# Kernel optimization log

Hardware: AMD Instinct MI355X
Metric: run time of the kernel (lower is better)

## Reference

```python
import jax, jax.numpy as jnp
import numpy as np

N_NODES = 50000
N_EDGES = 800000
IN_DIM = 13
HID = 64
LAYER_DIMS = [(IN_DIM, HID), (HID, HID), (HID, HID), (HID, HID), (HID, 1)]


def setup_inputs() -> dict:
    key = jax.random.key(0)
    ks = jax.random.split(key, 20)
    x = jax.random.normal(ks[0], (N_NODES, IN_DIM), dtype=jnp.float32)
    edge_index = jax.random.randint(ks[1], (2, N_EDGES), 0, N_NODES)
    edge_weight = jax.random.uniform(ks[2], (N_EDGES,), dtype=jnp.float32)
    inp = {"x": x, "edge_index": edge_index, "edge_weight": edge_weight}
    for i, (di, do) in enumerate(LAYER_DIMS):
        s = 1.0 / np.sqrt(di)
        inp[f"Wrel{i}"] = (jax.random.normal(ks[3 + 3 * i], (di, do)) * s).astype(jnp.float32)
        inp[f"brel{i}"] = jnp.zeros((do,), dtype=jnp.float32)
        inp[f"Wroot{i}"] = (jax.random.normal(ks[4 + 3 * i], (di, do)) * s).astype(jnp.float32)
    return inp


def _graph_conv(x, src, dst, ew, Wrel, brel, Wroot):
    # PyG GraphConv: out = lin_rel(sum_{j in N(i)} w_e * x_j) + lin_root(x_i)
    msgs = ew[:, None] * x[src]                      # [E, d_in] gather
    aggr = jax.ops.segment_sum(msgs, dst, num_segments=N_NODES)  # [N, d_in]
    return aggr @ Wrel + brel + x @ Wroot


def reference(x, edge_index, edge_weight,
              Wrel0, brel0, Wroot0,
              Wrel1, brel1, Wroot1,
              Wrel2, brel2, Wroot2,
              Wrel3, brel3, Wroot3,
              Wrel4, brel4, Wroot4):
    src, dst = edge_index[0], edge_index[1]  # source_to_target flow
    params = [
        (Wrel0, brel0, Wroot0),
        (Wrel1, brel1, Wroot1),
        (Wrel2, brel2, Wroot2),
        (Wrel3, brel3, Wroot3),
        (Wrel4, brel4, Wroot4),
    ]
    h = x
    for Wr, br, Ws in params[:-1]:
        h = jax.nn.relu(_graph_conv(h, src, dst, edge_weight, Wr, br, Ws))
    Wr, br, Ws = params[-1]
    h = _graph_conv(h, src, dst, edge_weight, Wr, br, Ws)
    return jax.nn.sigmoid(h)  # [N, 1]
```

## Files before the change

### kernel.cpp

```cpp
#include <hip/hip_runtime.h>
#include <math.h>

#define N_NODES 50000
#define N_EDGES 800000
#define NBUCKET 196
#define CHUNK 4096
#define NCHUNK 196
#define SCAN_N (NBUCKET * NCHUNK)
#define SB_A 151
#define SB_B 196
#define EPT 16
#define CAP_FINE 8192
#define MAXEPAD (N_EDGES + N_NODES * 4)

typedef __attribute__((ext_vector_type(8))) _Float16 f16x8;
typedef __attribute__((ext_vector_type(4))) float f32x4;

__device__ __forceinline__ int roundup4(int v) { return (v + 3) & ~3; }


__device__ __forceinline__ int block_excl_scan(int v, int* wsum) {
    int t = threadIdx.x, lane = t & 63, w = t >> 6;
    int sc = v;
    #pragma unroll
    for (int o = 1; o < 64; o <<= 1) {
        int u = __shfl_up(sc, o, 64);
        if (lane >= o) sc += u;
    }
    if (lane == 63) wsum[w] = sc;
    __syncthreads();
    int add = 0;
    #pragma unroll
    for (int j = 0; j < 4; ++j) if (j < w) add += wsum[j];
    return add + sc - v;
}


__global__ void hist_kernel(const int* __restrict__ dst, int* __restrict__ h,
                            int* __restrict__ counts,
                            const float* __restrict__ W1r, const float* __restrict__ W1o,
                            const float* __restrict__ W2r, const float* __restrict__ W2o,
                            const float* __restrict__ W3r, const float* __restrict__ W3o,
                            _Float16* __restrict__ wfrag) {
    if (blockIdx.x >= NCHUNK) {
        int b = blockIdx.x - NCHUNK, t = threadIdx.x;
        const float* Wr = (b == 0) ? W1r : (b == 1) ? W2r : W3r;
        const float* Wo = (b == 0) ? W1o : (b == 1) ? W2o : W3o;
        _Float16* out = wfrag + (size_t)b * 8192;
        for (int i = t; i < 1024; i += 256) {
            int frag = i >> 6, lane = i & 63;
            int m = frag >> 3, ct = (frag >> 1) & 3, ks = frag & 1;
            int col = ct * 16 + (lane & 15);
            int kb = ks * 32 + (lane >> 4) * 8;
            const float* W = m ? Wo : Wr;
            f16x8 v;
            #pragma unroll
            for (int j = 0; j < 8; ++j) v[j] = (_Float16)W[(kb + j) * 64 + col];
            *(f16x8*)&out[(size_t)i * 8] = v;
        }
        return;
    }
    __shared__ int hist[NBUCKET];
    for (int i = threadIdx.x; i < NBUCKET; i += 256) hist[i] = 0;
    __syncthreads();
    int base = blockIdx.x * CHUNK;
    int n = min(CHUNK, N_EDGES - base);
    for (int k = threadIdx.x; k < n; k += 256) {
        int d = dst[base + k];
        atomicAdd(&hist[d >> 8], 1);
        atomicAdd(&counts[d], 1);
    }
    __syncthreads();
    for (int i = threadIdx.x; i < NBUCKET; i += 256)
        h[i * NCHUNK + blockIdx.x] = hist[i];
}


__global__ void scan_blocks_dual(int* __restrict__ h, const int* __restrict__ counts,
                                 int* __restrict__ offs, int* __restrict__ blocksums) {
    __shared__ int wsum[4];
    int bid = blockIdx.x, t = threadIdx.x;
    if (bid < SB_A) {
        int i = bid * 256 + t;
        int v = (i < SCAN_N) ? h[i] : 0;
        int e = block_excl_scan(v, wsum);
        if (i < SCAN_N) h[i] = e;
        if (t == 255) blocksums[bid] = e + v;
    } else {
        int j = (bid - SB_A) * 256 + t;
        int v = (j < N_NODES) ? roundup4(counts[j]) : 0;
        int e = block_excl_scan(v, wsum);
        if (j < N_NODES) offs[j] = e;
        if (t == 255) blocksums[bid] = e + v;
    }
}

__global__ void scan_mid(const int* __restrict__ blocksums, int* __restrict__ blockoffs) {
    __shared__ int wsum[4];
    int base = (blockIdx.x == 0) ? 0 : SB_A;
    int n = (blockIdx.x == 0) ? SB_A : SB_B;
    int t = threadIdx.x;
    int v = (t < n) ? blocksums[base + t] : 0;
    int e = block_excl_scan(v, wsum);
    if (t < n) blockoffs[base + t] = e;
}

__global__ void scan_add_dual(int* __restrict__ h, int* __restrict__ offs,
                              const int* __restrict__ counts,
                              const int* __restrict__ blockoffs) {
    int bid = blockIdx.x, t = threadIdx.x;
    if (bid < SB_A) {
        int i = bid * 256 + t;
        if (i < SCAN_N) h[i] += blockoffs[bid];
    } else {
        int j = (bid - SB_A) * 256 + t;
        if (j < N_NODES) {
            int v = offs[j] + blockoffs[bid];
            offs[j] = v;
            if (j == N_NODES - 1) offs[N_NODES] = v + roundup4(counts[j]);
        }
    }
}


__launch_bounds__(256, 4)
__global__ void scatter_coarse(const int* __restrict__ src, const int* __restrict__ dst,
                               const float* __restrict__ ew, const int* __restrict__ hs,
                               int2* __restrict__ ecoarse) {
    __shared__ int cnt[NBUCKET];
    __shared__ int excl[NBUCKET];
    __shared__ int cur[NBUCKET];
    __shared__ int gbase[NBUCKET];
    __shared__ int wsum[4];
    __shared__ int2 stage[CHUNK];

    int t = threadIdx.x;
    int base = blockIdx.x * CHUNK;
    int n = min(CHUNK, N_EDGES - base);

    for (int i = t; i < NBUCKET; i += 256) {
        cnt[i] = 0;
        gbase[i] = hs[i * NCHUNK + blockIdx.x];
    }
    __syncthreads();

    int rx[EPT];
    float rw[EPT];
    #pragma unroll
    for (int j = 0; j < EPT; ++j) {
        int k = t + j * 256;
        if (k < n) {
            int e = base + k;
            int d = dst[e];
            rx[j] = (d << 16) | src[e];
            rw[j] = ew[e];
            atomicAdd(&cnt[d >> 8], 1);
        }
    }
    __syncthreads();

    {
        int v = (t < NBUCKET) ? cnt[t] : 0;
        int e = block_excl_scan(v, wsum);
        if (t < NBUCKET) { excl[t] = e; cur[t] = e; }
    }
    __syncthreads();

    #pragma unroll
    for (int j = 0; j < EPT; ++j) {
        int k = t + j * 256;
        if (k < n) {
            int b = ((unsigned)rx[j]) >> 24;
            int p = atomicAdd(&cur[b], 1);
            stage[p] = make_int2(rx[j], __float_as_int(rw[j]));
        }
    }
    __syncthreads();

    for (int k = t; k < n; k += 256) {
        int2 r = stage[k];
        int b = ((unsigned)r.x) >> 24;
        ecoarse[gbase[b] + (k - excl[b])] = r;
    }
}


__launch_bounds__(256)
__global__ void fine_sort(const int* __restrict__ h, const int* __restrict__ offs,
                          const int2* __restrict__ ecoarse, int2* __restrict__ esrt) {
    int b = blockIdx.x, t = threadIdx.x;
    __shared__ int cur[256];
    __shared__ int2 stage[CAP_FINE];
    int bstartU = h[b * NCHUNK];
    int bendU = (b == NBUCKET - 1) ? N_EDGES : h[(b + 1) * NCHUNK];
    int nbU = bendU - bstartU;
    int P = offs[b << 8];
    int nodeEnd = min((b + 1) << 8, N_NODES);
    int plen = offs[nodeEnd] - P;
    int dstv = (b << 8) + t;
    cur[t] = (dstv < N_NODES) ? offs[dstv] - P : 0;
    __syncthreads();
    if (plen <= CAP_FINE) {
        for (int k = t; k < plen; k += 256) stage[k] = make_int2(0, 0);
        __syncthreads();
        for (int k = t; k < nbU; k += 256) {
            int2 r = ecoarse[bstartU + k];
            int d = (((unsigned)r.x) >> 16) & 255;
            int p = atomicAdd(&cur[d], 1);
            stage[p] = make_int2(r.x & 0xFFFF, r.y);
        }
        __syncthreads();
        for (int k = t; k < plen; k += 256) esrt[P + k] = stage[k];
    } else {
        for (int k = t; k < plen; k += 256) esrt[P + k] = make_int2(0, 0);
        __syncthreads();
        for (int k = t; k < nbU; k += 256) {
            int2 r = ecoarse[bstartU + k];
            int d = (((unsigned)r.x) >> 16) & 255;
            int p = atomicAdd(&cur[d], 1);
            esrt[P + p] = make_int2(r.x & 0xFFFF, r.y);
        }
    }
}


__device__ __forceinline__ float bcast(float v, int k) {
    return __int_as_float(__builtin_amdgcn_readlane(__float_as_int(v), k));
}


__launch_bounds__(256)
__global__ void layer0_fused(const int* __restrict__ offs, const int2* __restrict__ esrt,
                             const float* __restrict__ x, const float* __restrict__ Wrel,
                             const float* __restrict__ bias, const float* __restrict__ Wroot,
                             _Float16* __restrict__ h0) {
    int wid = (blockIdx.x * blockDim.x + threadIdx.x) >> 6;
    int lane = threadIdx.x & 63;
    float wr[13], wo[13];
    #pragma unroll
    for (int k = 0; k < 13; ++k) {
        wr[k] = Wrel[k * 64 + lane];
        wo[k] = Wroot[k * 64 + lane];
    }
    float bc = bias[lane];
    int q = lane >> 4, f = lane & 15;
    int beg = offs[wid], end = offs[wid + 1];
    float acc = 0.f;
    bool fv = (f < 13);
    int i = beg + q;
    for (; i + 4 < end; i += 8) {
        int2 e0 = esrt[i], e1 = esrt[i + 4];
        float v0 = fv ? x[(size_t)e0.x * 13 + f] : 0.f;
        float v1 = fv ? x[(size_t)e1.x * 13 + f] : 0.f;
        acc = fmaf(__int_as_float(e0.y), v0, acc);
        acc = fmaf(__int_as_float(e1.y), v1, acc);
    }
    if (i < end) {
        int2 e = esrt[i];
        float v = fv ? x[(size_t)e.x * 13 + f] : 0.f;
        acc = fmaf(__int_as_float(e.y), v, acc);
    }
    acc += __shfl_xor(acc, 16, 64);
    acc += __shfl_xor(acc, 32, 64);
    float hv = (lane < 13) ? x[(size_t)wid * 13 + lane] : 0.f;
    float a0 = bc, a1 = 0.f, a2 = 0.f, a3 = 0.f;
    #pragma unroll
    for (int k = 0; k + 2 <= 13; k += 2) {
        a0 = fmaf(bcast(acc, k), wr[k], a0);
        a1 = fmaf(bcast(hv, k), wo[k], a1);
        a2 = fmaf(bcast(acc, k + 1), wr[k + 1], a2);
        a3 = fmaf(bcast(hv, k + 1), wo[k + 1], a3);
    }
    a0 = fmaf(bcast(acc, 12), wr[12], a0);
    a1 = fmaf(bcast(hv, 12), wo[12], a1);
    float o = fmaxf((a0 + a2) + (a1 + a3), 0.f);
    h0[(size_t)wid * 64 + lane] = (_Float16)o;
}


template <bool FINAL>
__launch_bounds__(256)
__global__ void layer_fused(const int* __restrict__ offs, const int2* __restrict__ esrt,
                            const _Float16* __restrict__ hin, const _Float16* __restrict__ wfrag_l,
                            const float* __restrict__ bias, _Float16* __restrict__ hout,
                            const float* __restrict__ Wrel4, const float* __restrict__ Wroot4,
                            float* __restrict__ z, float* __restrict__ root) {
    __shared__ __align__(16) _Float16 aggrHi[32][72];
    __shared__ __align__(16) _Float16 aggrLo[32][72];
    __shared__ float zpart[4][32], rpart[4][32];
    int t = threadIdx.x;
    int rowbase = blockIdx.x * 32;
    int w = t >> 6, lane = t & 63;

    f16x8 br0 = *(const f16x8*)&wfrag_l[(size_t)(((0 * 4 + w) * 2 + 0) * 64 + lane) * 8];
    f16x8 br1 = *(const f16x8*)&wfrag_l[(size_t)(((0 * 4 + w) * 2 + 1) * 64 + lane) * 8];
    f16x8 bo0 = *(const f16x8*)&wfrag_l[(size_t)(((1 * 4 + w) * 2 + 0) * 64 + lane) * 8];
    f16x8 bo1 = *(const f16x8*)&wfrag_l[(size_t)(((1 * 4 + w) * 2 + 1) * 64 + lane) * 8];
    int r = lane & 15, kq = lane >> 4;
    float bc = bias[w * 16 + r];
    float w4rv = 0.f, w4ov = 0.f;
    if (FINAL) { w4rv = Wrel4[w * 16 + r]; w4ov = Wroot4[w * 16 + r]; }

    int qw = t >> 4, l = t & 15;
    int hi8 = l >> 3, f8 = l & 7;
    #pragma unroll
    for (int rr = 0; rr < 2; ++rr) {
        int node = rowbase + qw + rr * 16;
        float a[8] = {0.f, 0.f, 0.f, 0.f, 0.f, 0.f, 0.f, 0.f};
        if (node < N_NODES) {
            int beg = offs[node], end = offs[node + 1];
            int i = beg;
            for (; i + 4 < end; i += 8) {
                int4 p0 = *(const int4*)(esrt + i);
                int4 p1 = *(const int4*)(esrt + i + 2);
                int4 p2 = *(const int4*)(esrt + i + 4);
                int4 p3 = *(const int4*)(esrt + i + 6);
                int s0 = hi8 ? p0.z : p0.x; float w0 = __int_as_float(hi8 ? p0.w : p0.y);
                int s1 = hi8 ? p1.z : p1.x; float w1 = __int_as_float(hi8 ? p1.w : p1.y);
                int s2 = hi8 ? p2.z : p2.x; float w2 = __int_as_float(hi8 ? p2.w : p2.y);
                int s3 = hi8 ? p3.z : p3.x; float w3 = __int_as_float(hi8 ? p3.w : p3.y);
                f16x8 r0 = *(const f16x8*)(hin + (size_t)s0 * 64 + f8 * 8);
                f16x8 r1 = *(const f16x8*)(hin + (size_t)s1 * 64 + f8 * 8);
                f16x8 r2 = *(const f16x8*)(hin + (size_t)s2 * 64 + f8 * 8);
                f16x8 r3 = *(const f16x8*)(hin + (size_t)s3 * 64 + f8 * 8);
                #pragma unroll
                for (int j = 0; j < 8; ++j) {
                    a[j] = fmaf(w0, (float)r0[j], a[j]);
                    a[j] = fmaf(w1, (float)r1[j], a[j]);
                    a[j] = fmaf(w2, (float)r2[j], a[j]);
                    a[j] = fmaf(w3, (float)r3[j], a[j]);
                }
            }
            if (i < end) {
                int4 p0 = *(const int4*)(esrt + i);
                int4 p1 = *(const int4*)(esrt + i + 2);
                int s0 = hi8 ? p0.z : p0.x; float w0 = __int_as_float(hi8 ? p0.w : p0.y);
                int s1 = hi8 ? p1.z : p1.x; float w1 = __int_as_float(hi8 ? p1.w : p1.y);
                f16x8 r0 = *(const f16x8*)(hin + (size_t)s0 * 64 + f8 * 8);
                f16x8 r1 = *(const f16x8*)(hin + (size_t)s1 * 64 + f8 * 8);
                #pragma unroll
                for (int j = 0; j < 8; ++j) {
                    a[j] = fmaf(w0, (float)r0[j], a[j]);
                    a[j] = fmaf(w1, (float)r1[j], a[j]);
                }
            }
        }
        #pragma unroll
        for (int j = 0; j < 8; ++j) a[j] += __shfl_xor(a[j], 8, 64);
        f16x8 wv;
        #pragma unroll
        for (int j = 0; j < 8; ++j) {
            _Float16 hh = (_Float16)a[j];
            wv[j] = hi8 ? (_Float16)(a[j] - (float)hh) : hh;
        }
        int row = qw + rr * 16;
        _Float16* dstp = hi8 ? &aggrLo[row][f8 * 8] : &aggrHi[row][f8 * 8];
        *(f16x8*)dstp = wv;
    }
    __syncthreads();

    #pragma unroll
    for (int g = 0; g < 2; ++g) {
        int lr = g * 16 + r;
        int grow = min(rowbase + lr, N_NODES - 1);
        f32x4 acc = {bc, bc, bc, bc};
        {
            f16x8 Ah = *(const f16x8*)&aggrHi[lr][0 * 32 + kq * 8];
            f16x8 Al = *(const f16x8*)&aggrLo[lr][0 * 32 + kq * 8];
            f16x8 Ar = *(const f16x8*)&hin[(size_t)grow * 64 + 0 * 32 + kq * 8];
            acc = __builtin_amdgcn_mfma_f32_16x16x32_f16(Ah, br0, acc, 0, 0, 0);
            acc = __builtin_amdgcn_mfma_f32_16x16x32_f16(Al, br0, acc, 0, 0, 0);
            acc = __builtin_amdgcn_mfma_f32_16x16x32_f16(Ar, bo0, acc, 0, 0, 0);
        }
        {
            f16x8 Ah = *(const f16x8*)&aggrHi[lr][1 * 32 + kq * 8];
            f16x8 Al = *(const f16x8*)&aggrLo[lr][1 * 32 + kq * 8];
            f16x8 Ar = *(const f16x8*)&hin[(size_t)grow * 64 + 1 * 32 + kq * 8];
            acc = __builtin_amdgcn_mfma_f32_16x16x32_f16(Ah, br1, acc, 0, 0, 0);
            acc = __builtin_amdgcn_mfma_f32_16x16x32_f16(Al, br1, acc, 0, 0, 0);
            acc = __builtin_amdgcn_mfma_f32_16x16x32_f16(Ar, bo1, acc, 0, 0, 0);
        }
        if (FINAL) {
            #pragma unroll
            for (int j = 0; j < 4; ++j) {
                float o = fmaxf(acc[j], 0.f);
                float zz = o * w4rv, rv = o * w4ov;
                #pragma unroll
                for (int m = 1; m < 16; m <<= 1) {
                    zz += __shfl_xor(zz, m, 64);
                    rv += __shfl_xor(rv, m, 64);
                }
                if (r == 0) {
                    int lrow = g * 16 + (lane >> 4) * 4 + j;
                    zpart[w][lrow] = zz;
                    rpart[w][lrow] = rv;
                }
            }
        } else {
            #pragma unroll
            for (int j = 0; j < 4; ++j) {
                int row = rowbase + g * 16 + (lane >> 4) * 4 + j;
                if (row < N_NODES)
                    hout[(size_t)row * 64 + w * 16 + r] = (_Float16)fmaxf(acc[j], 0.f);
            }
        }
    }
    if (FINAL) {
        __syncthreads();
        if (t < 32) {
            int row = rowbase + t;
            if (row < N_NODES) {
                z[row] = zpart[0][t] + zpart[1][t] + zpart[2][t] + zpart[3][t];
                root[row] = rpart[0][t] + rpart[1][t] + rpart[2][t] + rpart[3][t];
            }
        }
    }
}


__launch_bounds__(256)
__global__ void final_aggr(const int* __restrict__ offs, const int2* __restrict__ esrt,
                           const float* __restrict__ z, const float* __restrict__ root,
                           const float* __restrict__ b4, float* __restrict__ out) {
    int tid = blockIdx.x * blockDim.x + threadIdx.x;
    int node = tid >> 2, g = tid & 3;
    if (node >= N_NODES) return;
    int beg = offs[node], end = offs[node + 1];
    float a = 0.f;
    int i = beg + g;
    for (; i + 4 < end; i += 8) {
        int2 e0 = esrt[i], e1 = esrt[i + 4];
        a = fmaf(__int_as_float(e0.y), z[e0.x], a);
        a = fmaf(__int_as_float(e1.y), z[e1.x], a);
    }
    if (i < end) {
        int2 e = esrt[i];
        a = fmaf(__int_as_float(e.y), z[e.x], a);
    }
    a += __shfl_xor(a, 1, 64);
    a += __shfl_xor(a, 2, 64);
    if (g == 0) {
        float v = a + b4[0] + root[node];
        out[node] = 1.f / (1.f + expf(-v));
    }
}


extern "C" void kernel_launch(void* const* d_in, const int* in_sizes, int n_in,
                              void* d_out, int out_size, void* d_ws, size_t ws_size,
                              hipStream_t stream) {
    const float* x = (const float*)d_in[0];
    const int* eidx = (const int*)d_in[1];
    const float* ew = (const float*)d_in[2];
    const float* Wrel[5];
    const float* brel[5];
    const float* Wroot[5];
    for (int i = 0; i < 5; ++i) {
        Wrel[i] = (const float*)d_in[3 + 3 * i];
        brel[i] = (const float*)d_in[4 + 3 * i];
        Wroot[i] = (const float*)d_in[5 + 3 * i];
    }
    const int* src = eidx;
    const int* dst = eidx + N_EDGES;
    float* out = (float*)d_out;

    char* ws = (char*)d_ws;
    size_t off = 0;
    auto alloc = [&](size_t bytes) -> void* {
        void* p = ws + off;
        off = (off + bytes + 255) & ~(size_t)255;
        return p;
    };
    int* h = (int*)alloc((size_t)(SCAN_N + 256) * 4);
    int* blocksums = (int*)alloc(512 * 4);
    int* blockoffs = (int*)alloc(512 * 4);
    int* counts = (int*)alloc((size_t)N_NODES * 4);
    int* offs = (int*)alloc((size_t)(N_NODES + 1) * 4);
    int2* esrt = (int2*)alloc((size_t)MAXEPAD * 8);
    _Float16* h0 = (_Float16*)alloc((size_t)N_NODES * 64 * 2);
    _Float16* h1 = (_Float16*)alloc((size_t)N_NODES * 64 * 2);
    _Float16* wfrag = (_Float16*)alloc((size_t)3 * 8192 * 2);
    float* z = (float*)alloc((size_t)N_NODES * 4);
    float* root = (float*)alloc((size_t)N_NODES * 4);
    int2* ecoarse = (int2*)h0;
    (void)ws_size; (void)in_sizes; (void)n_in; (void)out_size;

    hipMemsetAsync(counts, 0, (size_t)N_NODES * 4, stream);
    hist_kernel<<<NCHUNK + 3, 256, 0, stream>>>(dst, h, counts,
                                                Wrel[1], Wroot[1], Wrel[2], Wroot[2],
                                                Wrel[3], Wroot[3], wfrag);
    scan_blocks_dual<<<SB_A + SB_B, 256, 0, stream>>>(h, counts, offs, blocksums);
    scan_mid<<<2, 256, 0, stream>>>(blocksums, blockoffs);
    scan_add_dual<<<SB_A + SB_B, 256, 0, stream>>>(h, offs, counts, blockoffs);
    scatter_coarse<<<NCHUNK, 256, 0, stream>>>(src, dst, ew, h, ecoarse);
    fine_sort<<<NBUCKET, 256, 0, stream>>>(h, offs, ecoarse, esrt);

    const int NODE_BLOCKS = N_NODES * 64 / 256;
    const int FB = (N_NODES + 31) / 32;

    layer0_fused<<<NODE_BLOCKS, 256, 0, stream>>>(offs, esrt, x, Wrel[0], brel[0], Wroot[0], h0);

    layer_fused<false><<<FB, 256, 0, stream>>>(offs, esrt, h0, wfrag, brel[1], h1,
                                               nullptr, nullptr, nullptr, nullptr);
    layer_fused<false><<<FB, 256, 0, stream>>>(offs, esrt, h1, wfrag + 8192, brel[2], h0,
                                               nullptr, nullptr, nullptr, nullptr);
    layer_fused<true><<<FB, 256, 0, stream>>>(offs, esrt, h0, wfrag + 16384, brel[3], nullptr,
                                              Wrel[4], Wroot[4], z, root);

    final_aggr<<<(N_NODES * 4 + 255) / 256, 256, 0, stream>>>(offs, esrt, z, root, brel[4], out);
}
```

Baseline: 181.9 us.

## Balance edge work across block threads and merge scan into reduce-then-scan

The three-kernel scan (block scan, mid scan, add) is replaced by two kernels. The first reduces each block to a sum, and the second rescans the block sums inside every block and then applies a local exclusive scan, which removes one launch. In the fused layer kernel, the block's 32-node edge range is split evenly across the 16 quarter-wave groups by 4-edge groups, rather than giving each group whole nodes. Partial sums are flushed into a shared fp32 tile with LDS atomics, which evens out load imbalance from skewed degrees but adds shared-memory atomics and a conversion pass.

```diff
diff --git a/kernel.cpp b/kernel.cpp
--- a/kernel.cpp
+++ b/kernel.cpp
@@ -9,6 +9,7 @@
 #define SCAN_N (NBUCKET * NCHUNK)
 #define SB_A 151
 #define SB_B 196
+#define NSB (SB_A + SB_B)
 #define EPT 16
 #define CAP_FINE 8192
 #define MAXEPAD (N_EDGES + N_NODES * 4)
@@ -76,48 +77,65 @@
 }
 
 
-__global__ void scan_blocks_dual(int* __restrict__ h, const int* __restrict__ counts,
-                                 int* __restrict__ offs, int* __restrict__ blocksums) {
+__global__ void scan_sums(const int* __restrict__ h, const int* __restrict__ counts,
+                          int* __restrict__ blocksums) {
     __shared__ int wsum[4];
     int bid = blockIdx.x, t = threadIdx.x;
+    int v;
     if (bid < SB_A) {
         int i = bid * 256 + t;
-        int v = (i < SCAN_N) ? h[i] : 0;
-        int e = block_excl_scan(v, wsum);
-        if (i < SCAN_N) h[i] = e;
-        if (t == 255) blocksums[bid] = e + v;
+        v = (i < SCAN_N) ? h[i] : 0;
     } else {
         int j = (bid - SB_A) * 256 + t;
-        int v = (j < N_NODES) ? roundup4(counts[j]) : 0;
-        int e = block_excl_scan(v, wsum);
-        if (j < N_NODES) offs[j] = e;
-        if (t == 255) blocksums[bid] = e + v;
-    }
-}
-
-__global__ void scan_mid(const int* __restrict__ blocksums, int* __restrict__ blockoffs) {
+        v = (j < N_NODES) ? roundup4(counts[j]) : 0;
+    }
+    int lane = t & 63, w = t >> 6;
+    int s = v;
+    #pragma unroll
+    for (int o = 1; o < 64; o <<= 1) s += __shfl_xor(s, o, 64);
+    if (lane == 0) wsum[w] = s;
+    __syncthreads();
+    if (t == 0) blocksums[bid] = wsum[0] + wsum[1] + wsum[2] + wsum[3];
+}
+
+__global__ void scan_apply(int* __restrict__ h, int* __restrict__ offs,
+                           const int* __restrict__ counts,
+                           const int* __restrict__ blocksums) {
+    __shared__ int sblk[NSB + 1];
     __shared__ int wsum[4];
-    int base = (blockIdx.x == 0) ? 0 : SB_A;
-    int n = (blockIdx.x == 0) ? SB_A : SB_B;
-    int t = threadIdx.x;
-    int v = (t < n) ? blocksums[base + t] : 0;
-    int e = block_excl_scan(v, wsum);
-    if (t < n) blockoffs[base + t] = e;
-}
-
-__global__ void scan_add_dual(int* __restrict__ h, int* __restrict__ offs,
-                              const int* __restrict__ counts,
-                              const int* __restrict__ blockoffs) {
     int bid = blockIdx.x, t = threadIdx.x;
+    if (t < 64) {
+        int carry = 0;
+        for (int c = 0; c < NSB; c += 64) {
+            int i = c + t;
+            int v = (i < NSB) ? blocksums[i] : 0;
+            int sc = v;
+            #pragma unroll
+            for (int o = 1; o < 64; o <<= 1) {
+                int u = __shfl_up(sc, o, 64);
+                if (t >= o) sc += u;
+            }
+            if (i < NSB) sblk[i] = carry + sc - v;
+            carry += __shfl(sc, 63, 64);
+        }
+        if (t == 0) sblk[NSB] = carry;
+    }
+    __syncthreads();
+    int v;
     if (bid < SB_A) {
         int i = bid * 256 + t;
-        if (i < SCAN_N) h[i] += blockoffs[bid];
+        v = (i < SCAN_N) ? h[i] : 0;
+        int e = block_excl_scan(v, wsum);
+        int base = sblk[bid];
+        if (i < SCAN_N) h[i] = e + base;
     } else {
         int j = (bid - SB_A) * 256 + t;
+        v = (j < N_NODES) ? roundup4(counts[j]) : 0;
+        int e = block_excl_scan(v, wsum);
+        int base = sblk[bid] - sblk[SB_A];
         if (j < N_NODES) {
-            int v = offs[j] + blockoffs[bid];
-            offs[j] = v;
-            if (j == N_NODES - 1) offs[N_NODES] = v + roundup4(counts[j]);
+            offs[j] = e + base;
+            if (j == N_NODES - 1) offs[N_NODES] = e + base + v;
         }
     }
 }
@@ -285,8 +303,10 @@
                             const float* __restrict__ bias, _Float16* __restrict__ hout,
                             const float* __restrict__ Wrel4, const float* __restrict__ Wroot4,
                             float* __restrict__ z, float* __restrict__ root) {
+    __shared__ __align__(16) float aggrF[32][68];
     __shared__ __align__(16) _Float16 aggrHi[32][72];
     __shared__ __align__(16) _Float16 aggrLo[32][72];
+    __shared__ int soffs[33];
     __shared__ float zpart[4][32], rpart[4][32];
     int t = threadIdx.x;
     int rowbase = blockIdx.x * 32;
@@ -301,61 +321,56 @@
     float w4rv = 0.f, w4ov = 0.f;
     if (FINAL) { w4rv = Wrel4[w * 16 + r]; w4ov = Wroot4[w * 16 + r]; }
 
+    if (t < 33) soffs[t] = offs[min(rowbase + t, N_NODES)];
+    for (int i = t; i < 32 * 68; i += 256) (&aggrF[0][0])[i] = 0.f;
+    __syncthreads();
+
     int qw = t >> 4, l = t & 15;
     int hi8 = l >> 3, f8 = l & 7;
-    #pragma unroll
-    for (int rr = 0; rr < 2; ++rr) {
-        int node = rowbase + qw + rr * 16;
+    int G0 = soffs[0];
+    int G = (soffs[32] - G0) >> 2;
+    int per = (G + 15) >> 4;
+    int gbeg = qw * per, gend = min(gbeg + per, G);
+    if (gbeg < gend) {
+        int ni = 0;
+        while (soffs[ni + 1] - G0 <= gbeg * 4) ++ni;
         float a[8] = {0.f, 0.f, 0.f, 0.f, 0.f, 0.f, 0.f, 0.f};
-        if (node < N_NODES) {
-            int beg = offs[node], end = offs[node + 1];
-            int i = beg;
-            for (; i + 4 < end; i += 8) {
-                int4 p0 = *(const int4*)(esrt + i);
-                int4 p1 = *(const int4*)(esrt + i + 2);
-                int4 p2 = *(const int4*)(esrt + i + 4);
-                int4 p3 = *(const int4*)(esrt + i + 6);
-                int s0 = hi8 ? p0.z : p0.x; float w0 = __int_as_float(hi8 ? p0.w : p0.y);
-                int s1 = hi8 ? p1.z : p1.x; float w1 = __int_as_float(hi8 ? p1.w : p1.y);
-                int s2 = hi8 ? p2.z : p2.x; float w2 = __int_as_float(hi8 ? p2.w : p2.y);
-                int s3 = hi8 ? p3.z : p3.x; float w3 = __int_as_float(hi8 ? p3.w : p3.y);
-                f16x8 r0 = *(const f16x8*)(hin + (size_t)s0 * 64 + f8 * 8);
-                f16x8 r1 = *(const f16x8*)(hin + (size_t)s1 * 64 + f8 * 8);
-                f16x8 r2 = *(const f16x8*)(hin + (size_t)s2 * 64 + f8 * 8);
-                f16x8 r3 = *(const f16x8*)(hin + (size_t)s3 * 64 + f8 * 8);
+        for (int g = gbeg; g < gend; ++g) {
+            if (g * 4 >= soffs[ni + 1] - G0) {
                 #pragma unroll
                 for (int j = 0; j < 8; ++j) {
-                    a[j] = fmaf(w0, (float)r0[j], a[j]);
-                    a[j] = fmaf(w1, (float)r1[j], a[j]);
-                    a[j] = fmaf(w2, (float)r2[j], a[j]);
-                    a[j] = fmaf(w3, (float)r3[j], a[j]);
+                    atomicAdd(&aggrF[ni][f8 * 8 + j], a[j]);
+                    a[j] = 0.f;
                 }
+                do { ++ni; } while (soffs[ni + 1] - G0 <= g * 4);
             }
-            if (i < end) {
-                int4 p0 = *(const int4*)(esrt + i);
-                int4 p1 = *(const int4*)(esrt + i + 2);
-                int s0 = hi8 ? p0.z : p0.x; float w0 = __int_as_float(hi8 ? p0.w : p0.y);
-                int s1 = hi8 ? p1.z : p1.x; float w1 = __int_as_float(hi8 ? p1.w : p1.y);
-                f16x8 r0 = *(const f16x8*)(hin + (size_t)s0 * 64 + f8 * 8);
-                f16x8 r1 = *(const f16x8*)(hin + (size_t)s1 * 64 + f8 * 8);
-                #pragma unroll
-                for (int j = 0; j < 8; ++j) {
-                    a[j] = fmaf(w0, (float)r0[j], a[j]);
-                    a[j] = fmaf(w1, (float)r1[j], a[j]);
-                }
+            int sbase = G0 + g * 4;
+            int4 p0 = *(const int4*)(esrt + sbase);
+            int4 p1 = *(const int4*)(esrt + sbase + 2);
+            int s0 = hi8 ? p0.z : p0.x; float w0 = __int_as_float(hi8 ? p0.w : p0.y);
+            int s1 = hi8 ? p1.z : p1.x; float w1 = __int_as_float(hi8 ? p1.w : p1.y);
+            f16x8 r0 = *(const f16x8*)(hin + (size_t)s0 * 64 + f8 * 8);
+            f16x8 r1 = *(const f16x8*)(hin + (size_t)s1 * 64 + f8 * 8);
+            #pragma unroll
+            for (int j = 0; j < 8; ++j) {
+                a[j] = fmaf(w0, (float)r0[j], a[j]);
+                a[j] = fmaf(w1, (float)r1[j], a[j]);
             }
         }
         #pragma unroll
-        for (int j = 0; j < 8; ++j) a[j] += __shfl_xor(a[j], 8, 64);
-        f16x8 wv;
+        for (int j = 0; j < 8; ++j) atomicAdd(&aggrF[ni][f8 * 8 + j], a[j]);
+    }
+    __syncthreads();
+
+    {
+        int row = t >> 3, c8 = (t & 7) * 8;
         #pragma unroll
         for (int j = 0; j < 8; ++j) {
-            _Float16 hh = (_Float16)a[j];
-            wv[j] = hi8 ? (_Float16)(a[j] - (float)hh) : hh;
-        }
-        int row = qw + rr * 16;
-        _Float16* dstp = hi8 ? &aggrLo[row][f8 * 8] : &aggrHi[row][f8 * 8];
-        *(f16x8*)dstp = wv;
+            float v = aggrF[row][c8 + j];
+            _Float16 hh = (_Float16)v;
+            aggrHi[row][c8 + j] = hh;
+            aggrLo[row][c8 + j] = (_Float16)(v - (float)hh);
+        }
     }
     __syncthreads();
 
@@ -473,7 +488,6 @@
     };
     int* h = (int*)alloc((size_t)(SCAN_N + 256) * 4);
     int* blocksums = (int*)alloc(512 * 4);
-    int* blockoffs = (int*)alloc(512 * 4);
     int* counts = (int*)alloc((size_t)N_NODES * 4);
     int* offs = (int*)alloc((size_t)(N_NODES + 1) * 4);
     int2* esrt = (int2*)alloc((size_t)MAXEPAD * 8);
@@ -489,9 +503,8 @@
     hist_kernel<<<NCHUNK + 3, 256, 0, stream>>>(dst, h, counts,
                                                 Wrel[1], Wroot[1], Wrel[2], Wroot[2],
                                                 Wrel[3], Wroot[3], wfrag);
-    scan_blocks_dual<<<SB_A + SB_B, 256, 0, stream>>>(h, counts, offs, blocksums);
-    scan_mid<<<2, 256, 0, stream>>>(blocksums, blockoffs);
-    scan_add_dual<<<SB_A + SB_B, 256, 0, stream>>>(h, offs, counts, blockoffs);
+    scan_sums<<<NSB, 256, 0, stream>>>(h, counts, blocksums);
+    scan_apply<<<NSB, 256, 0, stream>>>(h, offs, counts, blocksums);
     scatter_coarse<<<NCHUNK, 256, 0, stream>>>(src, dst, ew, h, ecoarse);
     fine_sort<<<NBUCKET, 256, 0, stream>>>(h, offs, ecoarse, esrt);
 
```

New measurement: 294.5 us. 1.62x slower.
